# Optimization experiments

Hardware: AMD Instinct MI355X
Metric: run time of the kernel (lower is better)

Reference implementation:

```python
import jax, jax.numpy as jnp
import numpy as np

D_MODEL = 512
N_HEADS = 8
D_HEAD = D_MODEL // N_HEADS


def setup_inputs() -> dict:
    key = jax.random.key(0)
    ks = jax.random.split(key, 10)
    B, N = 4, 2048
    s = 1.0 / np.sqrt(D_MODEL)
    inp = {
        'x': jax.random.normal(ks[0], (B, N, D_MODEL), jnp.float32),
        'attn_bias': jax.random.normal(ks[1], (B, 1, N, N), jnp.float32),
        'wq': jax.random.normal(ks[2], (D_MODEL, D_MODEL), jnp.float32) * s,
        'bq': jnp.zeros((D_MODEL,), jnp.float32),
        'wk': jax.random.normal(ks[3], (D_MODEL, D_MODEL), jnp.float32) * s,
        'bk': jnp.zeros((D_MODEL,), jnp.float32),
        'wv': jax.random.normal(ks[4], (D_MODEL, D_MODEL), jnp.float32) * s,
        'bv': jnp.zeros((D_MODEL,), jnp.float32),
        'wo': jax.random.normal(ks[5], (D_MODEL, D_MODEL), jnp.float32) * s,
        'bo': jnp.zeros((D_MODEL,), jnp.float32),
    }
    return inp


def reference(x, attn_bias, wq, bq, wk, bk, wv, bv, wo, bo):
    B, N, D = x.shape
    h, dh = N_HEADS, D_HEAD
    # projections; weights stored as (in, out) so y = x @ w + b
    q = (x @ wq + bq).reshape(B, N, h, dh).transpose(0, 2, 1, 3)  # (B,h,N,dh)
    k = (x @ wk + bk).reshape(B, N, h, dh).transpose(0, 2, 1, 3)
    v = (x @ wv + bv).reshape(B, N, h, dh).transpose(0, 2, 1, 3)
    scores = jnp.einsum('bhnd,bhmd->bhnm', q, k) / jnp.sqrt(jnp.float32(dh))
    scores = scores + attn_bias  # broadcast over heads
    attn = jax.nn.softmax(scores, axis=-1)
    out = jnp.einsum('bhnm,bhmd->bhnd', attn, v)
    out = out.transpose(0, 2, 1, 3).reshape(B, N, D)
    return out @ wo + bo
```

## Files before the change

kernel.cpp:

```cpp
#include <hip/hip_runtime.h>
#include <hip/hip_bf16.h>

typedef __bf16 bf16x8 __attribute__((ext_vector_type(8)));
typedef float f32x4 __attribute__((ext_vector_type(4)));
using u16 = unsigned short;
using u32 = unsigned int;

#define LDSS 72

__device__ __forceinline__ u16 f2bf(float f) {
  union { float f; u32 u; } v; v.f = f;
  u32 r = v.u + 0x7fffu + ((v.u >> 16) & 1u);
  return (u16)(r >> 16);
}

__device__ __forceinline__ u32 cvt_pk_bf16(float lo, float hi) {
  u32 r;
  asm("v_cvt_pk_bf16_f32 %0, %1, %2" : "=v"(r) : "v"(lo), "v"(hi));
  return r;
}

__global__ void cast_x_kernel(const float* __restrict__ x, u16* __restrict__ xb) {
  int i = (blockIdx.x * 256 + threadIdx.x) * 8;
  float4 f0 = *(const float4*)&x[i];
  float4 f1 = *(const float4*)&x[i + 4];
  u16 u[8];
  u[0] = f2bf(f0.x); u[1] = f2bf(f0.y); u[2] = f2bf(f0.z); u[3] = f2bf(f0.w);
  u[4] = f2bf(f1.x); u[5] = f2bf(f1.y); u[6] = f2bf(f1.z); u[7] = f2bf(f1.w);
  *(uint4*)&xb[i] = *(uint4*)u;
}

__global__ void cast_wT_kernel(const float* __restrict__ w0, const float* __restrict__ w1,
                               const float* __restrict__ w2, const float* __restrict__ w3,
                               u16* __restrict__ t0, u16* __restrict__ t1,
                               u16* __restrict__ t2, u16* __restrict__ t3) {
  int i = blockIdx.x * 256 + threadIdx.x;
  int wi = i >> 18;
  int r = i & 262143;
  int row = r >> 9, col = r & 511;
  const float* w; u16* t;
  if (wi == 0)      { w = w0; t = t0; }
  else if (wi == 1) { w = w1; t = t1; }
  else if (wi == 2) { w = w2; t = t2; }
  else              { w = w3; t = t3; }
  t[col * 512 + row] = f2bf(w[r]);
}

__global__ __launch_bounds__(256) void proj_kernel(
    const u16* __restrict__ xb,
    const u16* __restrict__ wqT, const u16* __restrict__ wkT, const u16* __restrict__ wvT,
    const float* __restrict__ bq, const float* __restrict__ bk, const float* __restrict__ bv,
    u16* __restrict__ Q, u16* __restrict__ K, u16* __restrict__ Vt) {
  __shared__ u16 Alds[64 * LDSS];
  __shared__ u16 Blds[64 * LDSS];
  int which = blockIdx.z;
  const u16* wT; const float* bias; u16* out;
  if (which == 0)      { wT = wqT; bias = bq; out = Q; }
  else if (which == 1) { wT = wkT; bias = bk; out = K; }
  else                 { wT = wvT; bias = bv; out = Vt; }

  int m0 = blockIdx.y * 64;
  int n0 = blockIdx.x * 64;
  int tid = threadIdx.x;
  int lane = tid & 63, w = tid >> 6;
  int wm = w >> 1, wn = w & 1;
  int l15 = lane & 15, l4 = lane >> 4;

  int r0 = tid >> 3, c8 = (tid & 7) * 8;

  uint4 ar0 = *(const uint4*)&xb[(m0 + r0) * 512 + c8];
  uint4 ar1 = *(const uint4*)&xb[(m0 + r0 + 32) * 512 + c8];
  uint4 br0 = *(const uint4*)&wT[(n0 + r0) * 512 + c8];
  uint4 br1 = *(const uint4*)&wT[(n0 + r0 + 32) * 512 + c8];

  f32x4 acc[2][2] = {};
  for (int ks = 0; ks < 8; ks++) {
    __syncthreads();
    *(uint4*)&Alds[r0 * LDSS + c8]        = ar0;
    *(uint4*)&Alds[(r0 + 32) * LDSS + c8] = ar1;
    *(uint4*)&Blds[r0 * LDSS + c8]        = br0;
    *(uint4*)&Blds[(r0 + 32) * LDSS + c8] = br1;
    __syncthreads();
    if (ks < 7) {
      int k0 = (ks + 1) * 64;
      ar0 = *(const uint4*)&xb[(m0 + r0) * 512 + k0 + c8];
      ar1 = *(const uint4*)&xb[(m0 + r0 + 32) * 512 + k0 + c8];
      br0 = *(const uint4*)&wT[(n0 + r0) * 512 + k0 + c8];
      br1 = *(const uint4*)&wT[(n0 + r0 + 32) * 512 + k0 + c8];
    }
#pragma unroll
    for (int kk = 0; kk < 2; kk++) {
      bf16x8 a[2], b[2];
#pragma unroll
      for (int f = 0; f < 2; f++) {
        a[f] = *(const bf16x8*)&Alds[(wm * 32 + f * 16 + l15) * LDSS + kk * 32 + l4 * 8];
        b[f] = *(const bf16x8*)&Blds[(wn * 32 + f * 16 + l15) * LDSS + kk * 32 + l4 * 8];
      }
#pragma unroll
      for (int fm = 0; fm < 2; fm++)
#pragma unroll
        for (int fn = 0; fn < 2; fn++) {
          if (which == 2)
            acc[fm][fn] = __builtin_amdgcn_mfma_f32_16x16x32_bf16(b[fn], a[fm], acc[fm][fn], 0, 0, 0);
          else
            acc[fm][fn] = __builtin_amdgcn_mfma_f32_16x16x32_bf16(a[fm], b[fn], acc[fm][fn], 0, 0, 0);
        }
    }
  }
  int bidx = m0 >> 11;
  int head = n0 >> 6;
  if (which == 2) {
#pragma unroll
    for (int fm = 0; fm < 2; fm++)
#pragma unroll
      for (int fn = 0; fn < 2; fn++)
#pragma unroll
        for (int r = 0; r < 4; r++) {
          int drow = wn * 32 + fn * 16 + l4 * 4 + r;
          int col  = wm * 32 + fm * 16 + l15;
          float vv = acc[fm][fn][r] + bias[n0 + drow];
          out[((size_t)(bidx * 8 + head) * 64 + drow) * 2048 + (m0 & 2047) + col] = f2bf(vv);
        }
  } else {
#pragma unroll
    for (int fm = 0; fm < 2; fm++)
#pragma unroll
      for (int fn = 0; fn < 2; fn++)
#pragma unroll
        for (int r = 0; r < 4; r++) {
          int row = wm * 32 + fm * 16 + l4 * 4 + r;
          int col = wn * 32 + fn * 16 + l15;
          int nrow = (m0 & 2047) + row;
          float vv = acc[fm][fn][r] + bias[n0 + col];
          out[(((size_t)(bidx * 8 + head) * 2048) + nrow) * 64 + col] = f2bf(vv);
        }
  }
}

__global__ __launch_bounds__(256, 4) void attn_kernel(
    const u16* __restrict__ Q, const u16* __restrict__ K, const u16* __restrict__ Vt,
    const float* __restrict__ bias, u16* __restrict__ O) {
  __shared__ u16 Klds[64 * LDSS];
  __shared__ u16 Vtlds[64 * LDSS];

  int qt = blockIdx.x, h = blockIdx.y, b = blockIdx.z;
  int tid = threadIdx.x;
  int lane = tid & 63, w = tid >> 6;
  int l15 = lane & 15, l4 = lane >> 4;
  int qrow = qt * 64 + w * 16 + l15;

  const u16* Qbh  = Q  + (size_t)(b * 8 + h) * 2048 * 64;
  const u16* Kbh  = K  + (size_t)(b * 8 + h) * 2048 * 64;
  const u16* Vtbh = Vt + (size_t)(b * 8 + h) * 64 * 2048;
  const float* biasrow = bias + (size_t)b * 2048 * 2048 + (size_t)qrow * 2048;

  bf16x8 aq[2];
#pragma unroll
  for (int kk = 0; kk < 2; kk++)
    aq[kk] = *(const bf16x8*)&Qbh[qrow * 64 + kk * 32 + l4 * 8];

  f32x4 o[4] = {};
  float mrow = -1e30f, lrow = 0.f;

  int srcA = (lane & 16) * 2 + l15;
  bool hiF = (l4 >> 1) != 0;

  int r0 = tid >> 3, c8 = (tid & 7) * 8;

  uint4 kr0 = *(const uint4*)&Kbh[r0 * 64 + c8];
  uint4 kr1 = *(const uint4*)&Kbh[(32 + r0) * 64 + c8];
  uint4 vr0 = *(const uint4*)&Vtbh[r0 * 2048 + c8];
  uint4 vr1 = *(const uint4*)&Vtbh[(r0 + 32) * 2048 + c8];
  float4 bb[4];
#pragma unroll
  for (int fj = 0; fj < 4; fj++)
    bb[fj] = *(const float4*)&biasrow[fj * 16 + l4 * 4];

  for (int t = 0; t < 32; t++) {
    __syncthreads();
    *(uint4*)&Klds[r0 * LDSS + c8]         = kr0;
    *(uint4*)&Klds[(r0 + 32) * LDSS + c8]  = kr1;
    *(uint4*)&Vtlds[r0 * LDSS + c8]        = vr0;
    *(uint4*)&Vtlds[(r0 + 32) * LDSS + c8] = vr1;
    __syncthreads();

    bool pf = (t < 31);
    float4 nbb[4];
    if (pf) {
      kr0 = *(const uint4*)&Kbh[((t + 1) * 64 + r0) * 64 + c8];
      kr1 = *(const uint4*)&Kbh[((t + 1) * 64 + 32 + r0) * 64 + c8];
      vr0 = *(const uint4*)&Vtbh[r0 * 2048 + (t + 1) * 64 + c8];
      vr1 = *(const uint4*)&Vtbh[(r0 + 32) * 2048 + (t + 1) * 64 + c8];
#pragma unroll
      for (int fj = 0; fj < 4; fj++)
        nbb[fj] = *(const float4*)&biasrow[(t + 1) * 64 + fj * 16 + l4 * 4];
    }

    f32x4 s[4] = {};
    __builtin_amdgcn_s_setprio(1);
#pragma unroll
    for (int kk = 0; kk < 2; kk++)
#pragma unroll
      for (int fj = 0; fj < 4; fj++) {
        bf16x8 kf = *(const bf16x8*)&Klds[(fj * 16 + l15) * LDSS + kk * 32 + l4 * 8];
        s[fj] = __builtin_amdgcn_mfma_f32_16x16x32_bf16(kf, aq[kk], s[fj], 0, 0, 0);
      }
    __builtin_amdgcn_s_setprio(0);

    float m = -1e30f;
#pragma unroll
    for (int fj = 0; fj < 4; fj++)
#pragma unroll
      for (int r = 0; r < 4; r++) {
        s[fj][r] = s[fj][r] * 0.125f + ((const float*)&bb[fj])[r];
        m = fmaxf(m, s[fj][r]);
      }
    m = fmaxf(m, __shfl_xor(m, 16));
    m = fmaxf(m, __shfl_xor(m, 32));

    if (!__all(m <= mrow + 8.0f)) {
      float mnew = fmaxf(mrow, m);
      float corr = __expf(mrow - mnew);
      mrow = mnew;
      lrow *= corr;
#pragma unroll
      for (int fo = 0; fo < 4; fo++)
#pragma unroll
        for (int r = 0; r < 4; r++) o[fo][r] *= corr;
    }

    u32 pk[4][2];
    float sum = 0.f;
#pragma unroll
    for (int fj = 0; fj < 4; fj++) {
      float p0 = __expf(s[fj][0] - mrow);
      float p1 = __expf(s[fj][1] - mrow);
      float p2 = __expf(s[fj][2] - mrow);
      float p3 = __expf(s[fj][3] - mrow);
      sum += (p0 + p1) + (p2 + p3);
      pk[fj][0] = cvt_pk_bf16(p0, p1);
      pk[fj][1] = cvt_pk_bf16(p2, p3);
    }
    sum += __shfl_xor(sum, 16);
    sum += __shfl_xor(sum, 32);
    lrow += sum;

#pragma unroll
    for (int kk = 0; kk < 2; kk++) {
      u32 a0 = __shfl((int)pk[2 * kk][0],     srcA);
      u32 b0 = __shfl((int)pk[2 * kk + 1][0], srcA);
      u32 a1 = __shfl((int)pk[2 * kk][1],     srcA);
      u32 b1 = __shfl((int)pk[2 * kk + 1][1], srcA);
      u32 a2 = __shfl((int)pk[2 * kk][0],     srcA + 16);
      u32 b2 = __shfl((int)pk[2 * kk + 1][0], srcA + 16);
      u32 a3 = __shfl((int)pk[2 * kk][1],     srcA + 16);
      u32 b3 = __shfl((int)pk[2 * kk + 1][1], srcA + 16);
      union { u32 u[4]; bf16x8 v; } pu;
      pu.u[0] = hiF ? b0 : a0;
      pu.u[1] = hiF ? b1 : a1;
      pu.u[2] = hiF ? b2 : a2;
      pu.u[3] = hiF ? b3 : a3;
      __builtin_amdgcn_s_setprio(1);
#pragma unroll
      for (int fo = 0; fo < 4; fo++) {
        bf16x8 vt = *(const bf16x8*)&Vtlds[(fo * 16 + l15) * LDSS + kk * 32 + l4 * 8];
        o[fo] = __builtin_amdgcn_mfma_f32_16x16x32_bf16(vt, pu.v, o[fo], 0, 0, 0);
      }
      __builtin_amdgcn_s_setprio(0);
    }

    if (pf) {
#pragma unroll
      for (int fj = 0; fj < 4; fj++) bb[fj] = nbb[fj];
    }
  }

  float inv = 1.0f / lrow;
  size_t obase = (size_t)(b * 2048 + qrow) * 512 + h * 64;
#pragma unroll
  for (int fo = 0; fo < 4; fo++) {
    u32 wlo = cvt_pk_bf16(o[fo][0] * inv, o[fo][1] * inv);
    u32 whi = cvt_pk_bf16(o[fo][2] * inv, o[fo][3] * inv);
    *(u32*)&O[obase + fo * 16 + l4 * 4]     = wlo;
    *(u32*)&O[obase + fo * 16 + l4 * 4 + 2] = whi;
  }
}

__global__ __launch_bounds__(256) void outproj_kernel(
    const u16* __restrict__ Ob, const u16* __restrict__ woT,
    const float* __restrict__ bo, float* __restrict__ out) {
  __shared__ u16 Alds[64 * LDSS];
  __shared__ u16 Blds[64 * LDSS];
  int m0 = blockIdx.y * 64;
  int n0 = blockIdx.x * 64;
  int tid = threadIdx.x;
  int lane = tid & 63, w = tid >> 6;
  int wm = w >> 1, wn = w & 1;
  int l15 = lane & 15, l4 = lane >> 4;

  int r0 = tid >> 3, c8 = (tid & 7) * 8;
  uint4 ar0 = *(const uint4*)&Ob[(m0 + r0) * 512 + c8];
  uint4 ar1 = *(const uint4*)&Ob[(m0 + r0 + 32) * 512 + c8];
  uint4 br0 = *(const uint4*)&woT[(n0 + r0) * 512 + c8];
  uint4 br1 = *(const uint4*)&woT[(n0 + r0 + 32) * 512 + c8];

  f32x4 acc[2][2] = {};
  for (int ks = 0; ks < 8; ks++) {
    __syncthreads();
    *(uint4*)&Alds[r0 * LDSS + c8]        = ar0;
    *(uint4*)&Alds[(r0 + 32) * LDSS + c8] = ar1;
    *(uint4*)&Blds[r0 * LDSS + c8]        = br0;
    *(uint4*)&Blds[(r0 + 32) * LDSS + c8] = br1;
    __syncthreads();
    if (ks < 7) {
      int k0 = (ks + 1) * 64;
      ar0 = *(const uint4*)&Ob[(m0 + r0) * 512 + k0 + c8];
      ar1 = *(const uint4*)&Ob[(m0 + r0 + 32) * 512 + k0 + c8];
      br0 = *(const uint4*)&woT[(n0 + r0) * 512 + k0 + c8];
      br1 = *(const uint4*)&woT[(n0 + r0 + 32) * 512 + k0 + c8];
    }
#pragma unroll
    for (int kk = 0; kk < 2; kk++) {
      bf16x8 a[2], bfr[2];
#pragma unroll
      for (int f = 0; f < 2; f++) {
        a[f] = *(const bf16x8*)&Alds[(wm * 32 + f * 16 + l15) * LDSS + kk * 32 + l4 * 8];
        bfr[f] = *(const bf16x8*)&Blds[(wn * 32 + f * 16 + l15) * LDSS + kk * 32 + l4 * 8];
      }
#pragma unroll
      for (int fm = 0; fm < 2; fm++)
#pragma unroll
        for (int fn = 0; fn < 2; fn++)
          acc[fm][fn] = __builtin_amdgcn_mfma_f32_16x16x32_bf16(a[fm], bfr[fn], acc[fm][fn], 0, 0, 0);
    }
  }
#pragma unroll
  for (int fm = 0; fm < 2; fm++)
#pragma unroll
    for (int fn = 0; fn < 2; fn++)
#pragma unroll
      for (int r = 0; r < 4; r++) {
        int row = wm * 32 + fm * 16 + l4 * 4 + r;
        int col = wn * 32 + fn * 16 + l15;
        out[(size_t)(m0 + row) * 512 + n0 + col] = acc[fm][fn][r] + bo[n0 + col];
      }
}

extern "C" void kernel_launch(void* const* d_in, const int* in_sizes, int n_in,
                              void* d_out, int out_size, void* d_ws, size_t ws_size,
                              hipStream_t stream) {
  const float* x    = (const float*)d_in[0];
  const float* bias = (const float*)d_in[1];
  const float* wq   = (const float*)d_in[2];
  const float* bq   = (const float*)d_in[3];
  const float* wk   = (const float*)d_in[4];
  const float* bk   = (const float*)d_in[5];
  const float* wv   = (const float*)d_in[6];
  const float* bv   = (const float*)d_in[7];
  const float* wo   = (const float*)d_in[8];
  const float* bo   = (const float*)d_in[9];
  float* out = (float*)d_out;

  char* ws = (char*)d_ws;
  u16* xb  = (u16*)(ws + 0);
  u16* wqT = (u16*)(ws + 8388608);
  u16* wkT = (u16*)(ws + 8912896);
  u16* wvT = (u16*)(ws + 9437184);
  u16* woT = (u16*)(ws + 9961472);
  u16* Qb  = (u16*)(ws + 10485760);
  u16* Kb  = (u16*)(ws + 18874368);
  u16* VtB = (u16*)(ws + 27262976);
  u16* Ob  = (u16*)(ws + 35651584);

  hipLaunchKernelGGL(cast_x_kernel, dim3(2048), dim3(256), 0, stream, x, xb);
  hipLaunchKernelGGL(cast_wT_kernel, dim3(4096), dim3(256), 0, stream,
                     wq, wk, wv, wo, wqT, wkT, wvT, woT);
  hipLaunchKernelGGL(proj_kernel, dim3(8, 128, 3), dim3(256), 0, stream,
                     xb, wqT, wkT, wvT, bq, bk, bv, Qb, Kb, VtB);
  hipLaunchKernelGGL(attn_kernel, dim3(32, 8, 4), dim3(256), 0, stream,
                     Qb, Kb, VtB, bias, Ob);
  hipLaunchKernelGGL(outproj_kernel, dim3(8, 128), dim3(256), 0, stream,
                     Ob, woT, bo, out);
}
```

Baseline: 149.3 us.

## Switch attention kernel to 32x32x16 MFMA with 128-row query tiles

Rewrites the attention inner loop to use 32x32x16 bf16 MFMA instead of 16x16x32, giving each wave 32 query rows and each block 128 rows, so the grid is halved. Each K/V tile loaded into LDS is now reused across twice as many queries, and the P-matrix reshuffle shrinks to a single xor-32 lane exchange. The bias prefetch moves later in the loop. In exchange, register use rises (launch bounds drop to 2 blocks per CU) and there are fewer blocks to spread across the CUs.

```diff
diff --git a/kernel.cpp b/kernel.cpp
--- a/kernel.cpp
+++ b/kernel.cpp
@@ -3,6 +3,7 @@
 
 typedef __bf16 bf16x8 __attribute__((ext_vector_type(8)));
 typedef float f32x4 __attribute__((ext_vector_type(4)));
+typedef float f32x16 __attribute__((ext_vector_type(16)));
 using u16 = unsigned short;
 using u32 = unsigned int;
 
@@ -137,7 +138,7 @@
   }
 }
 
-__global__ __launch_bounds__(256, 4) void attn_kernel(
+__global__ __launch_bounds__(256, 2) void attn_kernel(
     const u16* __restrict__ Q, const u16* __restrict__ K, const u16* __restrict__ Vt,
     const float* __restrict__ bias, u16* __restrict__ O) {
   __shared__ u16 Klds[64 * LDSS];
@@ -146,24 +147,21 @@
   int qt = blockIdx.x, h = blockIdx.y, b = blockIdx.z;
   int tid = threadIdx.x;
   int lane = tid & 63, w = tid >> 6;
-  int l15 = lane & 15, l4 = lane >> 4;
-  int qrow = qt * 64 + w * 16 + l15;
+  int l31 = lane & 31, hi = lane >> 5;
+  int qrow = qt * 128 + w * 32 + l31;
 
   const u16* Qbh  = Q  + (size_t)(b * 8 + h) * 2048 * 64;
   const u16* Kbh  = K  + (size_t)(b * 8 + h) * 2048 * 64;
   const u16* Vtbh = Vt + (size_t)(b * 8 + h) * 64 * 2048;
-  const float* biasrow = bias + (size_t)b * 2048 * 2048 + (size_t)qrow * 2048;
-
-  bf16x8 aq[2];
-#pragma unroll
-  for (int kk = 0; kk < 2; kk++)
-    aq[kk] = *(const bf16x8*)&Qbh[qrow * 64 + kk * 32 + l4 * 8];
-
-  f32x4 o[4] = {};
+  const float* biasq = bias + (size_t)b * 2048 * 2048 + (size_t)qrow * 2048;
+
+  bf16x8 qf[4];
+#pragma unroll
+  for (int dk = 0; dk < 4; dk++)
+    qf[dk] = *(const bf16x8*)&Qbh[qrow * 64 + dk * 16 + hi * 8];
+
+  f32x16 o[2] = {};
   float mrow = -1e30f, lrow = 0.f;
-
-  int srcA = (lane & 16) * 2 + l15;
-  bool hiF = (l4 >> 1) != 0;
 
   int r0 = tid >> 3, c8 = (tid & 7) * 8;
 
@@ -171,10 +169,12 @@
   uint4 kr1 = *(const uint4*)&Kbh[(32 + r0) * 64 + c8];
   uint4 vr0 = *(const uint4*)&Vtbh[r0 * 2048 + c8];
   uint4 vr1 = *(const uint4*)&Vtbh[(r0 + 32) * 2048 + c8];
-  float4 bb[4];
-#pragma unroll
-  for (int fj = 0; fj < 4; fj++)
-    bb[fj] = *(const float4*)&biasrow[fj * 16 + l4 * 4];
+  float4 bb[8];
+#pragma unroll
+  for (int kt = 0; kt < 2; kt++)
+#pragma unroll
+    for (int g = 0; g < 4; g++)
+      bb[kt * 4 + g] = *(const float4*)&biasq[kt * 32 + 8 * g + 4 * hi];
 
   for (int t = 0; t < 32; t++) {
     __syncthreads();
@@ -185,37 +185,37 @@
     __syncthreads();
 
     bool pf = (t < 31);
-    float4 nbb[4];
     if (pf) {
       kr0 = *(const uint4*)&Kbh[((t + 1) * 64 + r0) * 64 + c8];
       kr1 = *(const uint4*)&Kbh[((t + 1) * 64 + 32 + r0) * 64 + c8];
       vr0 = *(const uint4*)&Vtbh[r0 * 2048 + (t + 1) * 64 + c8];
       vr1 = *(const uint4*)&Vtbh[(r0 + 32) * 2048 + (t + 1) * 64 + c8];
-#pragma unroll
-      for (int fj = 0; fj < 4; fj++)
-        nbb[fj] = *(const float4*)&biasrow[(t + 1) * 64 + fj * 16 + l4 * 4];
-    }
-
-    f32x4 s[4] = {};
+    }
+
+    f32x16 s[2] = {};
     __builtin_amdgcn_s_setprio(1);
 #pragma unroll
-    for (int kk = 0; kk < 2; kk++)
-#pragma unroll
-      for (int fj = 0; fj < 4; fj++) {
-        bf16x8 kf = *(const bf16x8*)&Klds[(fj * 16 + l15) * LDSS + kk * 32 + l4 * 8];
-        s[fj] = __builtin_amdgcn_mfma_f32_16x16x32_bf16(kf, aq[kk], s[fj], 0, 0, 0);
-      }
+    for (int dk = 0; dk < 4; dk++) {
+      bf16x8 a0 = *(const bf16x8*)&Klds[l31 * LDSS + dk * 16 + hi * 8];
+      s[0] = __builtin_amdgcn_mfma_f32_32x32x16_bf16(a0, qf[dk], s[0], 0, 0, 0);
+      bf16x8 a1 = *(const bf16x8*)&Klds[(32 + l31) * LDSS + dk * 16 + hi * 8];
+      s[1] = __builtin_amdgcn_mfma_f32_32x32x16_bf16(a1, qf[dk], s[1], 0, 0, 0);
+    }
     __builtin_amdgcn_s_setprio(0);
 
     float m = -1e30f;
 #pragma unroll
-    for (int fj = 0; fj < 4; fj++)
-#pragma unroll
-      for (int r = 0; r < 4; r++) {
-        s[fj][r] = s[fj][r] * 0.125f + ((const float*)&bb[fj])[r];
-        m = fmaxf(m, s[fj][r]);
-      }
-    m = fmaxf(m, __shfl_xor(m, 16));
+    for (int kt = 0; kt < 2; kt++)
+#pragma unroll
+      for (int g = 0; g < 4; g++) {
+        float4 bv4 = bb[kt * 4 + g];
+#pragma unroll
+        for (int j = 0; j < 4; j++) {
+          float val = s[kt][g * 4 + j] * 0.125f + ((const float*)&bv4)[j];
+          s[kt][g * 4 + j] = val;
+          m = fmaxf(m, val);
+        }
+      }
     m = fmaxf(m, __shfl_xor(m, 32));
 
     if (!__all(m <= mrow + 8.0f)) {
@@ -224,66 +224,72 @@
       mrow = mnew;
       lrow *= corr;
 #pragma unroll
-      for (int fo = 0; fo < 4; fo++)
-#pragma unroll
-        for (int r = 0; r < 4; r++) o[fo][r] *= corr;
-    }
-
-    u32 pk[4][2];
+      for (int dt = 0; dt < 2; dt++)
+#pragma unroll
+        for (int i = 0; i < 16; i++) o[dt][i] *= corr;
+    }
+
+    u32 c[2][8];
     float sum = 0.f;
 #pragma unroll
-    for (int fj = 0; fj < 4; fj++) {
-      float p0 = __expf(s[fj][0] - mrow);
-      float p1 = __expf(s[fj][1] - mrow);
-      float p2 = __expf(s[fj][2] - mrow);
-      float p3 = __expf(s[fj][3] - mrow);
-      sum += (p0 + p1) + (p2 + p3);
-      pk[fj][0] = cvt_pk_bf16(p0, p1);
-      pk[fj][1] = cvt_pk_bf16(p2, p3);
-    }
-    sum += __shfl_xor(sum, 16);
+    for (int kt = 0; kt < 2; kt++)
+#pragma unroll
+      for (int g = 0; g < 4; g++) {
+        float p0 = __expf(s[kt][g * 4 + 0] - mrow);
+        float p1 = __expf(s[kt][g * 4 + 1] - mrow);
+        float p2 = __expf(s[kt][g * 4 + 2] - mrow);
+        float p3 = __expf(s[kt][g * 4 + 3] - mrow);
+        sum += (p0 + p1) + (p2 + p3);
+        c[kt][2 * g]     = cvt_pk_bf16(p0, p1);
+        c[kt][2 * g + 1] = cvt_pk_bf16(p2, p3);
+      }
     sum += __shfl_xor(sum, 32);
     lrow += sum;
 
-#pragma unroll
-    for (int kk = 0; kk < 2; kk++) {
-      u32 a0 = __shfl((int)pk[2 * kk][0],     srcA);
-      u32 b0 = __shfl((int)pk[2 * kk + 1][0], srcA);
-      u32 a1 = __shfl((int)pk[2 * kk][1],     srcA);
-      u32 b1 = __shfl((int)pk[2 * kk + 1][1], srcA);
-      u32 a2 = __shfl((int)pk[2 * kk][0],     srcA + 16);
-      u32 b2 = __shfl((int)pk[2 * kk + 1][0], srcA + 16);
-      u32 a3 = __shfl((int)pk[2 * kk][1],     srcA + 16);
-      u32 b3 = __shfl((int)pk[2 * kk + 1][1], srcA + 16);
-      union { u32 u[4]; bf16x8 v; } pu;
-      pu.u[0] = hiF ? b0 : a0;
-      pu.u[1] = hiF ? b1 : a1;
-      pu.u[2] = hiF ? b2 : a2;
-      pu.u[3] = hiF ? b3 : a3;
-      __builtin_amdgcn_s_setprio(1);
-#pragma unroll
-      for (int fo = 0; fo < 4; fo++) {
-        bf16x8 vt = *(const bf16x8*)&Vtlds[(fo * 16 + l15) * LDSS + kk * 32 + l4 * 8];
-        o[fo] = __builtin_amdgcn_mfma_f32_16x16x32_bf16(vt, pu.v, o[fo], 0, 0, 0);
-      }
-      __builtin_amdgcn_s_setprio(0);
-    }
+    u32 dx[2][8];
+#pragma unroll
+    for (int kt = 0; kt < 2; kt++)
+#pragma unroll
+      for (int j = 0; j < 8; j++)
+        dx[kt][j] = (u32)__shfl_xor((int)c[kt][j], 32);
 
     if (pf) {
 #pragma unroll
-      for (int fj = 0; fj < 4; fj++) bb[fj] = nbb[fj];
-    }
+      for (int kt = 0; kt < 2; kt++)
+#pragma unroll
+        for (int g = 0; g < 4; g++)
+          bb[kt * 4 + g] = *(const float4*)&biasq[(t + 1) * 64 + kt * 32 + 8 * g + 4 * hi];
+    }
+
+    __builtin_amdgcn_s_setprio(1);
+#pragma unroll
+    for (int kk = 0; kk < 4; kk++) {
+      const int kt = kk >> 1, jA = 4 * (kk & 1);
+      union { u32 u[4]; bf16x8 v; } pfg;
+      pfg.u[0] = hi ? dx[kt][jA + 2] : c[kt][jA];
+      pfg.u[1] = hi ? dx[kt][jA + 3] : c[kt][jA + 1];
+      pfg.u[2] = hi ? c[kt][jA + 2]  : dx[kt][jA];
+      pfg.u[3] = hi ? c[kt][jA + 3]  : dx[kt][jA + 1];
+#pragma unroll
+      for (int dt = 0; dt < 2; dt++) {
+        bf16x8 va = *(const bf16x8*)&Vtlds[(dt * 32 + l31) * LDSS + kk * 16 + hi * 8];
+        o[dt] = __builtin_amdgcn_mfma_f32_32x32x16_bf16(va, pfg.v, o[dt], 0, 0, 0);
+      }
+    }
+    __builtin_amdgcn_s_setprio(0);
   }
 
   float inv = 1.0f / lrow;
   size_t obase = (size_t)(b * 2048 + qrow) * 512 + h * 64;
 #pragma unroll
-  for (int fo = 0; fo < 4; fo++) {
-    u32 wlo = cvt_pk_bf16(o[fo][0] * inv, o[fo][1] * inv);
-    u32 whi = cvt_pk_bf16(o[fo][2] * inv, o[fo][3] * inv);
-    *(u32*)&O[obase + fo * 16 + l4 * 4]     = wlo;
-    *(u32*)&O[obase + fo * 16 + l4 * 4 + 2] = whi;
-  }
+  for (int dt = 0; dt < 2; dt++)
+#pragma unroll
+    for (int g = 0; g < 4; g++) {
+      uint2 pr;
+      pr.x = cvt_pk_bf16(o[dt][4 * g + 0] * inv, o[dt][4 * g + 1] * inv);
+      pr.y = cvt_pk_bf16(o[dt][4 * g + 2] * inv, o[dt][4 * g + 3] * inv);
+      *(uint2*)&O[obase + dt * 32 + 8 * g + 4 * hi] = pr;
+    }
 }
 
 __global__ __launch_bounds__(256) void outproj_kernel(
@@ -377,7 +383,7 @@
                      wq, wk, wv, wo, wqT, wkT, wvT, woT);
   hipLaunchKernelGGL(proj_kernel, dim3(8, 128, 3), dim3(256), 0, stream,
                      xb, wqT, wkT, wvT, bq, bk, bv, Qb, Kb, VtB);
-  hipLaunchKernelGGL(attn_kernel, dim3(32, 8, 4), dim3(256), 0, stream,
+  hipLaunchKernelGGL(attn_kernel, dim3(16, 8, 4), dim3(256), 0, stream,
                      Qb, Kb, VtB, bias, Ob);
   hipLaunchKernelGGL(outproj_kernel, dim3(8, 128), dim3(256), 0, stream,
                      Ob, woT, bo, out);
```

Measured after the change: 139.8 us. 1.07x faster.
